# Optimization experiments

Measured on AMD Instinct MI355X. Metric: run time of the kernel, lower is better.

The kernel has to match this reference:

```python
import jax, jax.numpy as jnp
import numpy as np

T, D_IN, D_OUT, HEADS, FREQ = 2048, 1024, 1024, 8, 10000
DH = D_OUT // HEADS


def absolute_pos(t, d, freq):
    # AP[pos, 2i] = sin(pos / freq**(2i/d)), AP[pos, 2i+1] = cos(...); t even -> all cols filled
    pos = jnp.arange(t, dtype=jnp.float32)[:, None]            # [T,1]
    i = jnp.arange(t // 2, dtype=jnp.float32)[None, :]         # [1,T/2]
    angle = pos / (freq ** (2.0 * i / d))                      # [T,T/2]
    return jnp.stack([jnp.sin(angle), jnp.cos(angle)], axis=-1).reshape(t, t)


def setup_inputs() -> dict:
    key = jax.random.key(0)
    ks = jax.random.split(key, 6)
    s = 0.02
    return {
        "x": jax.random.normal(ks[0], (T, D_IN), jnp.float32),
        "Wq": jax.random.normal(ks[1], (HEADS, DH, D_IN), jnp.float32) * s,
        "Wk": jax.random.normal(ks[2], (HEADS, DH, D_IN), jnp.float32) * s,
        "Wv": jax.random.normal(ks[3], (HEADS, DH, D_IN), jnp.float32) * s,
        "Wout2": jax.random.normal(ks[4], (DH, DH + 2), jnp.float32) * s,
        "Wout": jax.random.normal(ks[5], (D_IN, D_OUT), jnp.float32) * s,
    }


def reference(x, Wq, Wk, Wv, Wout2, Wout):
    t = x.shape[0]
    # diversity = 1 - cosine similarity (F.normalize with eps=1e-12)
    x_unit = x / jnp.maximum(jnp.linalg.norm(x, axis=1, keepdims=True), 1e-12)
    diversity = 1.0 - x_unit @ x_unit.T                        # [T,T]

    # all heads vectorized; torch Linear weight is [out,in] -> x @ W.T
    Q = jnp.einsum('td,hed->hte', x, Wq)                       # [H,T,DH]
    K = jnp.einsum('td,hed->hte', x, Wk)
    V = jnp.einsum('td,hed->hte', x, Wv)

    AP = absolute_pos(t, D_IN, FREQ)                           # [T,T]
    energies = jnp.einsum('hte,hse->hts', Q, K) + AP           # [H,T,T]

    att = jax.nn.softmax(energies, axis=-1)
    logp = jax.nn.log_softmax(energies, axis=-1)
    entropy = -(att * logp).sum(-1) / np.float32(np.log(t))    # [H,T]
    entropy = entropy / jnp.maximum(jnp.abs(entropy).sum(-1, keepdims=True), 1e-12)

    # dep_factor[j] broadcast over rows: masked[i,j] = dep[j]*att[i,j]
    dep = (diversity[None] * att).sum(-1) / diversity.sum(-1)[None]  # [H,T]
    att_win = att + dep[:, None, :] * att                      # [H,T,T]

    # dropout(p=0.5) treated as identity (eval mode)
    y = jnp.einsum('hts,hse->hte', att_win, V)                 # [H,T,DH]

    chars = jax.lax.stop_gradient(jnp.stack([entropy, dep], axis=-1))  # [H,T,2]
    y_s = jnp.einsum('htf,of->hto', jnp.concatenate([y, chars], axis=-1), Wout2)  # [H,T,DH]

    y_cat = jnp.transpose(y_s, (1, 0, 2)).reshape(t, D_OUT)    # cat heads along feature dim
    out = y_cat @ Wout.T                                       # [T,D_IN]
    return out, att_win[-1]
```

## Files before the change

### kernel.cpp

```cpp
#include <hip/hip_runtime.h>
#include <math.h>

#define TT  2048
#define NH  8
#define DH  128
#define LNT 7.6246189861593985f

typedef unsigned short ushort_t;
typedef __bf16 bf16x8 __attribute__((ext_vector_type(8)));
typedef _Float16 f16x8 __attribute__((ext_vector_type(8)));
typedef float f32x4 __attribute__((ext_vector_type(4)));
typedef unsigned int uintx4 __attribute__((ext_vector_type(4)));

#define MFMA16(a, b, c)  __builtin_amdgcn_mfma_f32_16x16x32_bf16(a, b, c, 0, 0, 0)
#define MFMA16F(a, b, c) __builtin_amdgcn_mfma_f32_16x16x32_f16(a, b, c, 0, 0, 0)

__device__ __forceinline__ bf16x8 ld8(const ushort_t* p) {
  uintx4 v = *(const uintx4*)p;
  return __builtin_bit_cast(bf16x8, v);
}
__device__ __forceinline__ f16x8 ld8f(const ushort_t* p) {
  uintx4 v = *(const uintx4*)p;
  return __builtin_bit_cast(f16x8, v);
}
__device__ __forceinline__ ushort_t f2bf(float x) {
  unsigned u = __float_as_uint(x);
  return (ushort_t)((u + 0x7fffu + ((u >> 16) & 1u)) >> 16);
}
__device__ __forceinline__ float bf2f(ushort_t b) {
  return __uint_as_float(((unsigned)b) << 16);
}
__device__ __forceinline__ ushort_t f2h(float x) {
  return __builtin_bit_cast(ushort_t, (_Float16)x);
}
__device__ __forceinline__ float h2f(ushort_t b) {
  return (float)__builtin_bit_cast(_Float16, b);
}


enum : size_t {
  F_XF   = 0u,
  F_UF   = 1048576u,
  F_QF   = 2097152u,
  F_KF   = 3145728u,
  F_VBF  = 4194304u,
  F_VT   = 5242880u,
  F_YCF  = 6291456u,
  F_WCAT = 7340032u,
  F_WOF  = 9437184u,
  F_DIVS = 9961472u,
  F_LST  = 9979904u,
  F_ENTR = 9996288u,
  F_ENT  = 10012672u,
  F_DEP  = 10029056u,
  F_W2F  = 10307584u,
  F_APH  = 10485760u,
  F_C    = 12582912u,
  F_LP   = 6291456u,
  F_SAP  = 6422528u,
  F_SCP  = 6553600u,
  F_E    = 16777216u,
  F_YPALL= 33554432u,
  F_YSH  = 2097152u,
};

__device__ __forceinline__ float blockReduceSum256(float v) {
  __shared__ float sh[4];
  #pragma unroll
  for (int m = 1; m < 64; m <<= 1) v += __shfl_xor(v, m, 64);
  if ((threadIdx.x & 63) == 0) sh[threadIdx.x >> 6] = v;
  __syncthreads();
  float r = sh[0] + sh[1] + sh[2] + sh[3];
  __syncthreads();
  return r;
}

__global__ __launch_bounds__(256) void k_pre(
    const float* __restrict__ x, const float* __restrict__ Wq,
    const float* __restrict__ Wk, const float* __restrict__ Wv,
    const float* __restrict__ Wo, const float* __restrict__ W2,
    ushort_t* __restrict__ xf, ushort_t* __restrict__ Wcat,
    ushort_t* __restrict__ Wof, ushort_t* __restrict__ W2f,
    ushort_t* __restrict__ Uf, ushort_t* __restrict__ APf) {
  int b = blockIdx.x;
  if (b < 6240) {
    int i = b * 256 + threadIdx.x;
    if (i < 1572864) {
      const float* src; ushort_t* dst; int j;
      if (i < 524288)       { src = x;  dst = xf;             j = i; }
      else if (i < 786432)  { src = Wq; dst = Wcat;           j = i - 524288; }
      else if (i < 1048576) { src = Wk; dst = Wcat + 1048576; j = i - 786432; }
      else if (i < 1310720) { src = Wv; dst = Wcat + 2097152; j = i - 1048576; }
      else                  { src = Wo; dst = Wof;            j = i - 1310720; }
      float4 v = ((const float4*)src)[j];
      uint2 w;
      w.x = (unsigned)f2h(v.x) | ((unsigned)f2h(v.y) << 16);
      w.y = (unsigned)f2h(v.z) | ((unsigned)f2h(v.w) << 16);
      ((uint2*)dst)[j] = w;
    } else {
      int idx = i - 1572864;
      int o = idx / 192, c = idx % 192;
      W2f[idx] = (c < 130) ? f2h(W2[o * 130 + c]) : (ushort_t)0;
    }
  } else if (b < 8288) {
    int t = b - 6240;
    const float* xr = x + (size_t)t * 1024;
    float ss = 0.f;
    for (int d = threadIdx.x; d < 1024; d += 256) { float v = xr[d]; ss += v * v; }
    ss = blockReduceSum256(ss);
    float inv = 1.f / fmaxf(sqrtf(ss), 1e-12f);
    for (int d = threadIdx.x; d < 1024; d += 256)
      Uf[(size_t)t * 1024 + d] = f2h(xr[d] * inv);
  } else {
    int bb = b - 8288;
    int tile_t = bb >> 4, sub = bb & 15;
    int base = sub * 2048;
    for (int u0 = threadIdx.x; u0 < 2048; u0 += 256) {
      int u = base + u0;
      int tile_s = u >> 8, slot = u & 255;
      int lg = slot >> 6, l15 = (slot >> 2) & 15, r = slot & 3;
      int t = tile_t * 16 + lg * 4 + r;
      int s = tile_s * 16 + l15;
      int i = s >> 1;
      float invf = __expf((float)i * -0.017988946039016016f);
      float ang = (float)t * invf;
      APf[(size_t)tile_t * 32768 + u] = f2h((s & 1) ? cosf(ang) : sinf(ang));
    }
  }
}

template <int MODE>
__device__ __forceinline__ void gemm_tile(
    ushort_t* As, ushort_t* Bs,
    const ushort_t* A, const ushort_t* B,
    float* Df, ushort_t* Dh,
    ushort_t* Dq, ushort_t* Dk, ushort_t* Dv,
    int M, int N, int K, int m0, int n0) {
  int tid = threadIdx.x, lane = tid & 63, w = tid >> 6;
  int l15 = lane & 15, lg = lane >> 4;
  int wr = w >> 1, wc = w & 1;

  const ushort_t* ga[4];
  const ushort_t* gb[4];
  ushort_t* la[4];
  ushort_t* lb[4];
  #pragma unroll
  for (int j = 0; j < 4; j++) {
    int u = (4 * w + j) * 64 + lane;
    int row = u >> 3;
    int kc8 = (u & 7) ^ (row & 7);
    ga[j] = A + (size_t)(m0 + row) * K + kc8 * 8;
    gb[j] = B + (size_t)(n0 + row) * K + kc8 * 8;
    la[j] = As + (4 * w + j) * 512;
    lb[j] = Bs + (4 * w + j) * 512;
  }

  f32x4 acc[4][4];
  #pragma unroll
  for (int i = 0; i < 4; i++)
    #pragma unroll
    for (int ct = 0; ct < 4; ct++) acc[i][ct] = (f32x4)0.f;

  for (int k0 = 0; k0 < K; k0 += 64) {
    __syncthreads();
    #pragma unroll
    for (int j = 0; j < 4; j++) {
      __builtin_amdgcn_global_load_lds(
          (const __attribute__((address_space(1))) void*)(ga[j] + k0),
          (__attribute__((address_space(3))) void*)la[j], 16, 0, 0);
      __builtin_amdgcn_global_load_lds(
          (const __attribute__((address_space(1))) void*)(gb[j] + k0),
          (__attribute__((address_space(3))) void*)lb[j], 16, 0, 0);
    }
    __syncthreads();
    #pragma unroll
    for (int kc = 0; kc < 2; kc++) {
      f16x8 af[4], bfr[4];
      #pragma unroll
      for (int i = 0; i < 4; i++) {
        int ra = wr * 64 + i * 16 + l15;
        af[i] = ld8f(As + (ra * 8 + ((kc * 4 + lg) ^ (ra & 7))) * 8);
        int rb = wc * 64 + i * 16 + l15;
        bfr[i] = ld8f(Bs + (rb * 8 + ((kc * 4 + lg) ^ (rb & 7))) * 8);
      }
      #pragma unroll
      for (int i = 0; i < 4; i++)
        #pragma unroll
        for (int ct = 0; ct < 4; ct++)
          acc[i][ct] = MFMA16F(af[i], bfr[ct], acc[i][ct]);
    }
  }
  #pragma unroll
  for (int i = 0; i < 4; i++) {
    #pragma unroll
    for (int ct = 0; ct < 4; ct++) {
      if (MODE == 5) {
        size_t tile_t = (size_t)(m0 + wr * 64 + i * 16) >> 4;
        size_t tile_s = (size_t)(n0 + wc * 64 + ct * 16) >> 4;
        uint2 wv;
        wv.x = (unsigned)f2bf(acc[i][ct][0]) | ((unsigned)f2bf(acc[i][ct][1]) << 16);
        wv.y = (unsigned)f2bf(acc[i][ct][2]) | ((unsigned)f2bf(acc[i][ct][3]) << 16);
        *(uint2*)(Dh + (tile_t * (size_t)(N >> 4) + tile_s) * 256 + lg * 64 + l15 * 4) = wv;
      } else {
        #pragma unroll
        for (int r = 0; r < 4; r++) {
          size_t mm = m0 + wr * 64 + i * 16 + lg * 4 + r;
          size_t nn = n0 + wc * 64 + ct * 16 + l15;
          float v = acc[i][ct][r];
          if (MODE == 0) Df[mm * N + nn] = v;
          if (MODE == 3) {
            if (nn < 1024) Dq[mm * 1024 + nn] = f2h(v);
            else if (nn < 2048) Dk[mm * 1024 + nn - 1024] = f2h(v);
            else Dv[mm * 1024 + nn - 2048] = f2bf(v);
          }
          if (MODE == 4) {
            size_t hh = mm >> 11, tt2 = mm & 2047;
            Dh[tt2 * 1024 + hh * 128 + nn] = f2h(v);
          }
        }
      }
    }
  }
}

template <int MODE>
__global__ __launch_bounds__(256) void k_gemm(
    const ushort_t* __restrict__ A, const ushort_t* __restrict__ B,
    float* __restrict__ Df, ushort_t* __restrict__ Dh,
    int M, int N, int K) {
  __shared__ __align__(16) ushort_t As[128 * 64];
  __shared__ __align__(16) ushort_t Bs[128 * 64];
  gemm_tile<MODE>(As, Bs, A, B, Df, Dh, nullptr, nullptr, nullptr,
                  M, N, K, blockIdx.y * 128, blockIdx.x * 128);
}

__global__ __launch_bounds__(256) void k_cqkv(
    const ushort_t* __restrict__ Uf, const ushort_t* __restrict__ xf,
    const ushort_t* __restrict__ Wcat,
    ushort_t* __restrict__ Cf, ushort_t* __restrict__ Qf,
    ushort_t* __restrict__ Kf, ushort_t* __restrict__ Vbf) {
  __shared__ __align__(16) ushort_t As[128 * 64];
  __shared__ __align__(16) ushort_t Bs[128 * 64];
  int bid = blockIdx.x;
  if (bid < 256) {
    gemm_tile<5>(As, Bs, Uf, Uf, nullptr, Cf, nullptr, nullptr, nullptr,
                 TT, TT, 1024, (bid >> 4) * 128, (bid & 15) * 128);
  } else {
    int b = bid - 256;
    gemm_tile<3>(As, Bs, xf, Wcat, nullptr, nullptr, Qf, Kf, Vbf,
                 TT, 3072, 1024, (b / 24) * 128, (b % 24) * 128);
  }
}

__global__ __launch_bounds__(256) void k_divsumf(const ushort_t* __restrict__ Cf,
                                                 float* __restrict__ divsum) {
  int tile_t = blockIdx.x;
  int tid = threadIdx.x;
  #pragma unroll
  for (int lg = 0; lg < 4; lg++) {
    float rs0 = 0.f, rs1 = 0.f, rs2 = 0.f, rs3 = 0.f;
    for (int u = tid; u < 128 * 8; u += 256) {
      int tile_s = u >> 3, j = u & 7;
      uintx4 v = *(const uintx4*)(Cf + ((size_t)tile_t * 128 + tile_s) * 256 + lg * 64 + j * 8);
      rs0 += bf2f((ushort_t)(v[0] & 0xffffu)) + bf2f((ushort_t)(v[2] & 0xffffu));
      rs1 += bf2f((ushort_t)(v[0] >> 16))     + bf2f((ushort_t)(v[2] >> 16));
      rs2 += bf2f((ushort_t)(v[1] & 0xffffu)) + bf2f((ushort_t)(v[3] & 0xffffu));
      rs3 += bf2f((ushort_t)(v[1] >> 16))     + bf2f((ushort_t)(v[3] >> 16));
    }
    float t0 = blockReduceSum256(rs0);
    float t1 = blockReduceSum256(rs1);
    float t2 = blockReduceSum256(rs2);
    float t3 = blockReduceSum256(rs3);
    if (tid == 0) {
      divsum[tile_t * 16 + lg * 4 + 0] = (float)TT - t0;
      divsum[tile_t * 16 + lg * 4 + 1] = (float)TT - t1;
      divsum[tile_t * 16 + lg * 4 + 2] = (float)TT - t2;
      divsum[tile_t * 16 + lg * 4 + 3] = (float)TT - t3;
    }
  }
}

__global__ __launch_bounds__(512, 4) void k_phase1m(
    const ushort_t* __restrict__ Qf, const ushort_t* __restrict__ Kf,
    const ushort_t* __restrict__ APf, const ushort_t* __restrict__ Cf,
    ushort_t* __restrict__ Ef,
    float* __restrict__ Lp, float* __restrict__ sap, float* __restrict__ scp) {
  int h = blockIdx.y, z = blockIdx.z;
  int tid = threadIdx.x, lane = tid & 63, w = tid >> 6;
  int l15 = lane & 15, lg = lane >> 4;
  int rowbase = blockIdx.x * 128 + w * 16;
  int s_begin = z * 256, s_end = s_begin + 256;
  __shared__ __align__(16) ushort_t Ks[64 * 128];

  f16x8 q[4];
  {
    const ushort_t* qp = Qf + (size_t)(rowbase + l15) * 1024 + h * DH + lg * 8;
    #pragma unroll
    for (int kc = 0; kc < 4; kc++) q[kc] = ld8f(qp + kc * 32);
  }
  const ushort_t* apb = APf + (size_t)(rowbase >> 4) * 32768 + lane * 4;
  const ushort_t* cfb = Cf  + (size_t)(rowbase >> 4) * 32768 + lane * 4;
  ushort_t* eb = Ef + ((size_t)(h * 128 + (rowbase >> 4)) * 128) * 256 + lane * 4;

  int n0 = w * 128 + lane;
  int sr0 = n0 >> 4, su0 = n0 & 15, sr1 = sr0 + 4;
  int wo0 = sr0 * 128 + ((su0 ^ (sr0 & 7)) * 8);
  int wo1 = sr1 * 128 + ((su0 ^ (sr1 & 7)) * 8);
  const ushort_t* kg0 = Kf + (size_t)sr0 * 1024 + h * DH + su0 * 8;
  const ushort_t* kg1 = Kf + (size_t)sr1 * 1024 + h * DH + su0 * 8;

  float Lv[4], sae[4], snc[4];
  #pragma unroll
  for (int r = 0; r < 4; r++) { Lv[r] = 0.f; sae[r] = 0.f; snc[r] = 0.f; }

  uintx4 ka = *(const uintx4*)(kg0 + (size_t)s_begin * 1024);
  uintx4 kb = *(const uintx4*)(kg1 + (size_t)s_begin * 1024);

  for (int s0 = s_begin; s0 < s_end; s0 += 64) {
    int ts0 = s0 >> 4;
    f32x4 acc[4];
    float cc[4][4];
    #pragma unroll
    for (int ct = 0; ct < 4; ct++) {
      uint2 ap2 = *(const uint2*)(apb + (size_t)(ts0 + ct) * 256);
      uint2 c2  = *(const uint2*)(cfb + (size_t)(ts0 + ct) * 256);
      acc[ct][0] = h2f((ushort_t)(ap2.x & 0xffffu));
      acc[ct][1] = h2f((ushort_t)(ap2.x >> 16));
      acc[ct][2] = h2f((ushort_t)(ap2.y & 0xffffu));
      acc[ct][3] = h2f((ushort_t)(ap2.y >> 16));
      cc[ct][0] = bf2f((ushort_t)(c2.x & 0xffffu));
      cc[ct][1] = bf2f((ushort_t)(c2.x >> 16));
      cc[ct][2] = bf2f((ushort_t)(c2.y & 0xffffu));
      cc[ct][3] = bf2f((ushort_t)(c2.y >> 16));
    }
    __syncthreads();
    *(uintx4*)(Ks + wo0) = ka;
    *(uintx4*)(Ks + wo1) = kb;
    int s1 = s0 + 64;
    if (s1 < s_end) {
      ka = *(const uintx4*)(kg0 + (size_t)s1 * 1024);
      kb = *(const uintx4*)(kg1 + (size_t)s1 * 1024);
    }
    __syncthreads();
    #pragma unroll
    for (int ct = 0; ct < 4; ct++) {
      int row = ct * 16 + l15, rb = row * 128, rs = row & 7;
      #pragma unroll
      for (int kc = 0; kc < 4; kc++) {
        f16x8 b = ld8f(Ks + rb + (((kc * 4 + lg) ^ rs) * 8));
        acc[ct] = MFMA16F(q[kc], b, acc[ct]);
      }
    }
    #pragma unroll
    for (int ct = 0; ct < 4; ct++) {
      uint2 ev;
      ev.x = (unsigned)f2h(acc[ct][0]) | ((unsigned)f2h(acc[ct][1]) << 16);
      ev.y = (unsigned)f2h(acc[ct][2]) | ((unsigned)f2h(acc[ct][3]) << 16);
      *(uint2*)(eb + (size_t)(ts0 + ct) * 256) = ev;
    }
    #pragma unroll
    for (int r = 0; r < 4; r++) {
      float e0 = acc[0][r], e1 = acc[1][r], e2 = acc[2][r], e3 = acc[3][r];
      float p0 = __expf(e0), p1 = __expf(e1), p2 = __expf(e2), p3 = __expf(e3);
      Lv[r]  += (p0 + p1) + (p2 + p3);
      sae[r] += (p0 * e0 + p1 * e1) + (p2 * e2 + p3 * e3);
      snc[r] += (p0 * cc[0][r] + p1 * cc[1][r]) + (p2 * cc[2][r] + p3 * cc[3][r]);
    }
  }
  #pragma unroll
  for (int r = 0; r < 4; r++) {
    #pragma unroll
    for (int m = 1; m < 16; m <<= 1) {
      Lv[r]  += __shfl_xor(Lv[r], m, 64);
      sae[r] += __shfl_xor(sae[r], m, 64);
      snc[r] += __shfl_xor(snc[r], m, 64);
    }
  }
  if (l15 == 0) {
    #pragma unroll
    for (int r = 0; r < 4; r++) {
      int t = rowbase + lg * 4 + r;
      size_t idx = (size_t)z * (NH * TT) + h * TT + t;
      Lp[idx] = Lv[r]; sap[idx] = sae[r]; scp[idx] = snc[r];
    }
  }
}

__global__ __launch_bounds__(256) void k_combine(
    const float* __restrict__ Lp, const float* __restrict__ sap,
    const float* __restrict__ scp, const float* __restrict__ divsum,
    float* __restrict__ Lst, float* __restrict__ entraw, float* __restrict__ dep) {
  int i = blockIdx.x * 256 + threadIdx.x;
  if (i >= NH * TT) return;
  float L = 0.f, sa = 0.f, sc = 0.f;
  #pragma unroll
  for (int c = 0; c < 8; c++) {
    size_t idx = (size_t)c * (NH * TT) + i;
    L += Lp[idx]; sa += sap[idx]; sc += scp[idx];
  }
  float logL = __logf(L);
  Lst[i] = logL;
  entraw[i] = (logL - sa / L) * (1.0f / LNT);
  int t = i & (TT - 1);
  dep[i] = (1.f - sc / L) / divsum[t];
}

__global__ __launch_bounds__(256) void k_entnorm(const float* __restrict__ entraw,
                                                 float* __restrict__ ent) {
  int h = blockIdx.x;
  float s = 0.f;
  for (int t = threadIdx.x; t < TT; t += 256) s += fabsf(entraw[h * TT + t]);
  s = blockReduceSum256(s);
  float inv = 1.f / fmaxf(s, 1e-12f);
  for (int t = threadIdx.x; t < TT; t += 256) ent[h * TT + t] = entraw[h * TT + t] * inv;
}

__global__ __launch_bounds__(256) void k_vprime(const ushort_t* __restrict__ Vbf,
                                                const float* __restrict__ dep,
                                                ushort_t* __restrict__ VT) {
  int h = blockIdx.y, s0 = blockIdx.x * 64;
  __shared__ float tile[64][130];
  int tid = threadIdx.x;
  for (int idx = tid; idx < 64 * 64; idx += 256) {
    int r = idx >> 6, c2 = (idx & 63) * 2;
    unsigned u = *(const unsigned*)&Vbf[(size_t)(s0 + r) * 1024 + h * DH + c2];
    tile[r][c2] = bf2f((ushort_t)(u & 0xffffu));
    tile[r][c2 + 1] = bf2f((ushort_t)(u >> 16));
  }
  __syncthreads();
  int e = tid >> 1, sh = (tid & 1) * 32;
  #pragma unroll
  for (int g = 0; g < 8; g++) {
    int sb = sh + g * 4;
    float v0 = tile[sb + 0][e] * (1.f + dep[h * TT + s0 + sb + 0]);
    float v1 = tile[sb + 1][e] * (1.f + dep[h * TT + s0 + sb + 1]);
    float v2 = tile[sb + 2][e] * (1.f + dep[h * TT + s0 + sb + 2]);
    float v3 = tile[sb + 3][e] * (1.f + dep[h * TT + s0 + sb + 3]);
    uint2 wv;
    wv.x = (unsigned)f2bf(v0) | ((unsigned)f2bf(v1) << 16);
    wv.y = (unsigned)f2bf(v2) | ((unsigned)f2bf(v3) << 16);
    *(uint2*)&VT[(size_t)(h * DH + e) * TT + s0 + sb] = wv;
  }
}

__global__ __launch_bounds__(512, 4) void k_phase2m(
    const ushort_t* __restrict__ Ef, const ushort_t* __restrict__ VT,
    const float* __restrict__ Lst, const float* __restrict__ dep,
    ushort_t* __restrict__ ypall, float* __restrict__ out2) {
  int h = (blockIdx.y + 7) & 7;
  int z = blockIdx.z;
  int tid = threadIdx.x, lane = tid & 63, w = tid >> 6;
  int l15 = lane & 15, lg = lane >> 4;
  int rowbase = blockIdx.x * 128 + w * 16;
  bool last = (h == NH - 1);
  int s_begin = z * 256, s_end = s_begin + 256;
  ushort_t* yp = ypall + (size_t)z * 2097152;

  __shared__ __align__(16) ushort_t Vs[128 * 64];
  __shared__ __align__(16) ushort_t Pst[8][16][72];

  float ml[4];
  #pragma unroll
  for (int r = 0; r < 4; r++) ml[r] = Lst[h * TT + rowbase + lg * 4 + r];
  const ushort_t* eb = Ef + ((size_t)(h * 128 + (rowbase >> 4)) * 128) * 256 + lane * 4;

  int n0 = w * 128 + lane;
  int ve0 = n0 >> 3, vu0 = n0 & 7;
  int vwo0 = ve0 * 64 + ((vu0 ^ (ve0 & 7)) * 8);
  int vwo1 = vwo0 + 512;
  const ushort_t* vg0 = VT + (size_t)(h * DH + ve0) * TT + vu0 * 8;
  const ushort_t* vg1 = vg0 + (size_t)8 * TT;

  f32x4 yacc[8];
  #pragma unroll
  for (int et = 0; et < 8; et++) yacc[et] = (f32x4)0.f;

  uintx4 va = *(const uintx4*)(vg0 + s_begin);
  uintx4 vb = *(const uintx4*)(vg1 + s_begin);

  for (int s0 = s_begin; s0 < s_end; s0 += 64) {
    int ts0 = s0 >> 4;
    uint2 e2[4];
    #pragma unroll
    for (int ct = 0; ct < 4; ct++)
      e2[ct] = *(const uint2*)(eb + (size_t)(ts0 + ct) * 256);
    __syncthreads();
    *(uintx4*)(Vs + vwo0) = va;
    *(uintx4*)(Vs + vwo1) = vb;
    int s1 = s0 + 64;
    if (s1 < s_end) {
      va = *(const uintx4*)(vg0 + s1);
      vb = *(const uintx4*)(vg1 + s1);
    }
    __syncthreads();
    float dv[4];
    if (last) {
      #pragma unroll
      for (int ct = 0; ct < 4; ct++) dv[ct] = dep[(NH - 1) * TT + s0 + ct * 16 + l15];
    }
    #pragma unroll
    for (int ct = 0; ct < 4; ct++) {
      float e0 = h2f((ushort_t)(e2[ct].x & 0xffffu));
      float e1 = h2f((ushort_t)(e2[ct].x >> 16));
      float e3 = h2f((ushort_t)(e2[ct].y & 0xffffu));
      float e4 = h2f((ushort_t)(e2[ct].y >> 16));
      float a0 = __expf(e0 - ml[0]);
      float a1 = __expf(e1 - ml[1]);
      float a2 = __expf(e3 - ml[2]);
      float a3 = __expf(e4 - ml[3]);
      Pst[w][lg * 4 + 0][ct * 16 + l15] = f2bf(a0);
      Pst[w][lg * 4 + 1][ct * 16 + l15] = f2bf(a1);
      Pst[w][lg * 4 + 2][ct * 16 + l15] = f2bf(a2);
      Pst[w][lg * 4 + 3][ct * 16 + l15] = f2bf(a3);
      if (last) {
        float sc = 1.f + dv[ct];
        out2[(size_t)(rowbase + lg * 4 + 0) * TT + s0 + ct * 16 + l15] = a0 * sc;
        out2[(size_t)(rowbase + lg * 4 + 1) * TT + s0 + ct * 16 + l15] = a1 * sc;
        out2[(size_t)(rowbase + lg * 4 + 2) * TT + s0 + ct * 16 + l15] = a2 * sc;
        out2[(size_t)(rowbase + lg * 4 + 3) * TT + s0 + ct * 16 + l15] = a3 * sc;
      }
    }
    asm volatile("" ::: "memory");
    #pragma unroll
    for (int c = 0; c < 2; c++) {
      bf16x8 ap = *(const bf16x8*)&Pst[w][l15][c * 32 + lg * 8];
      #pragma unroll
      for (int et = 0; et < 8; et++) {
        int e = et * 16 + l15;
        bf16x8 bv = ld8(Vs + e * 64 + (((c * 4 + lg) ^ (l15 & 7)) * 8));
        yacc[et] = MFMA16(ap, bv, yacc[et]);
      }
    }
    asm volatile("" ::: "memory");
  }
  #pragma unroll
  for (int et = 0; et < 8; et++)
    #pragma unroll
    for (int r = 0; r < 4; r++)
      yp[((size_t)h * TT + rowbase + lg * 4 + r) * DH + et * 16 + l15] = f2h(yacc[et][r]);
}

__device__ __forceinline__ void acc8(const ushort_t* p, float* s) {
  uintx4 v = *(const uintx4*)p;
  #pragma unroll
  for (int q = 0; q < 4; q++) {
    s[q * 2]     += h2f((ushort_t)(v[q] & 0xffffu));
    s[q * 2 + 1] += h2f((ushort_t)(v[q] >> 16));
  }
}
__global__ __launch_bounds__(256) void k_ysum(
    const ushort_t* __restrict__ ypall,
    const float* __restrict__ ent, const float* __restrict__ dep,
    ushort_t* __restrict__ ysh) {
  int i = blockIdx.x * 256 + threadIdx.x;
  int g = i & 15, t = (i >> 4) & 2047, h = i >> 15;
  size_t src = ((size_t)h * TT + t) * DH + g * 8;
  float s[8];
  #pragma unroll
  for (int q = 0; q < 8; q++) s[q] = 0.f;
  #pragma unroll
  for (int b = 0; b < 8; b++) acc8(ypall + (size_t)b * 2097152 + src, s);
  uintx4 o;
  o[0] = (unsigned)f2h(s[0]) | ((unsigned)f2h(s[1]) << 16);
  o[1] = (unsigned)f2h(s[2]) | ((unsigned)f2h(s[3]) << 16);
  o[2] = (unsigned)f2h(s[4]) | ((unsigned)f2h(s[5]) << 16);
  o[3] = (unsigned)f2h(s[6]) | ((unsigned)f2h(s[7]) << 16);
  ushort_t* row = ysh + ((size_t)h * TT + t) * 192;
  *(uintx4*)(row + g * 8) = o;
  if (g == 0) {
    uint2 cz;
    cz.x = (unsigned)f2h(ent[h * TT + t]) | ((unsigned)f2h(dep[h * TT + t]) << 16);
    cz.y = 0u;
    *(uint2*)(row + 128) = cz;
    uint2 z2; z2.x = 0u; z2.y = 0u;
    #pragma unroll
    for (int q = 132; q < 192; q += 4) *(uint2*)(row + q) = z2;
  }
}

extern "C" void kernel_launch(void* const* d_in, const int* in_sizes, int n_in,
                              void* d_out, int out_size, void* d_ws, size_t ws_size,
                              hipStream_t stream) {
  const float* x  = (const float*)d_in[0];
  const float* Wq = (const float*)d_in[1];
  const float* Wk = (const float*)d_in[2];
  const float* Wv = (const float*)d_in[3];
  const float* W2 = (const float*)d_in[4];
  const float* Wo = (const float*)d_in[5];
  float* out  = (float*)d_out;
  float* out2 = out + (size_t)TT * 1024;
  float* ws = (float*)d_ws;

  ushort_t* xf   = (ushort_t*)(ws + F_XF);
  ushort_t* Uf   = (ushort_t*)(ws + F_UF);
  ushort_t* Qf   = (ushort_t*)(ws + F_QF);
  ushort_t* Kf   = (ushort_t*)(ws + F_KF);
  ushort_t* Vbf  = (ushort_t*)(ws + F_VBF);
  ushort_t* VT   = (ushort_t*)(ws + F_VT);
  ushort_t* ycf  = (ushort_t*)(ws + F_YCF);
  ushort_t* Wcat = (ushort_t*)(ws + F_WCAT);
  ushort_t* Wof  = (ushort_t*)(ws + F_WOF);
  ushort_t* W2f  = (ushort_t*)(ws + F_W2F);
  ushort_t* APf  = (ushort_t*)(ws + F_APH);
  ushort_t* ysh  = (ushort_t*)(ws + F_YSH);
  ushort_t* Cf   = (ushort_t*)(ws + F_C);
  ushort_t* Ef   = (ushort_t*)(ws + F_E);
  ushort_t* ypall= (ushort_t*)(ws + F_YPALL);
  float* divsum = ws + F_DIVS;
  float* Lst    = ws + F_LST;
  float* entraw = ws + F_ENTR;
  float* ent    = ws + F_ENT;
  float* dep    = ws + F_DEP;
  float* Lp     = ws + F_LP;
  float* sap    = ws + F_SAP;
  float* scp    = ws + F_SCP;

  k_pre<<<10336, 256, 0, stream>>>(x, Wq, Wk, Wv, Wo, W2,
                                   xf, Wcat, Wof, W2f, Uf, APf);
  k_cqkv<<<640, 256, 0, stream>>>(Uf, xf, Wcat, Cf, Qf, Kf, Vbf);
  k_divsumf<<<128, 256, 0, stream>>>(Cf, divsum);

  k_phase1m<<<dim3(16, NH, 8), 512, 0, stream>>>(Qf, Kf, APf, Cf, Ef, Lp, sap, scp);
  k_combine<<<64, 256, 0, stream>>>(Lp, sap, scp, divsum, Lst, entraw, dep);
  k_entnorm<<<NH, 256, 0, stream>>>(entraw, ent);
  k_vprime<<<dim3(32, NH), 256, 0, stream>>>(Vbf, dep, VT);
  k_phase2m<<<dim3(16, NH, 8), 512, 0, stream>>>(Ef, VT, Lst, dep, ypall, out2);
  k_ysum<<<1024, 256, 0, stream>>>(ypall, ent, dep, ysh);
  k_gemm<4><<<dim3(1, 128), 256, 0, stream>>>(ysh, W2f, nullptr, ycf, 16384, 128, 192);
  k_gemm<0><<<dim3(8, 16), 256, 0, stream>>>(ycf, Wof, out, nullptr, TT, 1024, 1024);
}
```

Baseline: 174.1 us.

## Store unnormalized exp scores in phase1 and fuse diversity row sums into GEMM epilogue

Phase 1 now writes exp(energy) as bf16 instead of raw fp16 energies. Phase 2 therefore skips the second exponential and just copies these values into shared memory, applying 1/L once to the output accumulator and to the last-head attention output. The separate divsum kernel is removed: k_pre initialises divsum to T, and the cosine-similarity GEMM epilogue subtracts row sums atomically. This drops a kernel launch and a pass over C, but relies on unnormalized exp not overflowing bf16, and atomics make the summation order nondeterministic.

```diff
diff --git a/kernel.cpp b/kernel.cpp
--- a/kernel.cpp
+++ b/kernel.cpp
@@ -49,17 +49,17 @@
   F_WCAT = 7340032u,
   F_WOF  = 9437184u,
   F_DIVS = 9961472u,
-  F_LST  = 9979904u,
   F_ENTR = 9996288u,
   F_ENT  = 10012672u,
   F_DEP  = 10029056u,
+  F_LINV = 10045440u,
   F_W2F  = 10307584u,
   F_APH  = 10485760u,
   F_C    = 12582912u,
   F_LP   = 6291456u,
   F_SAP  = 6422528u,
   F_SCP  = 6553600u,
-  F_E    = 16777216u,
+  F_P    = 16777216u,
   F_YPALL= 33554432u,
   F_YSH  = 2097152u,
 };
@@ -81,7 +81,8 @@
     const float* __restrict__ Wo, const float* __restrict__ W2,
     ushort_t* __restrict__ xf, ushort_t* __restrict__ Wcat,
     ushort_t* __restrict__ Wof, ushort_t* __restrict__ W2f,
-    ushort_t* __restrict__ Uf, ushort_t* __restrict__ APf) {
+    ushort_t* __restrict__ Uf, ushort_t* __restrict__ APf,
+    float* __restrict__ divsum) {
   int b = blockIdx.x;
   if (b < 6240) {
     int i = b * 256 + threadIdx.x;
@@ -111,7 +112,7 @@
     float inv = 1.f / fmaxf(sqrtf(ss), 1e-12f);
     for (int d = threadIdx.x; d < 1024; d += 256)
       Uf[(size_t)t * 1024 + d] = f2h(xr[d] * inv);
-  } else {
+  } else if (b < 10336) {
     int bb = b - 8288;
     int tile_t = bb >> 4, sub = bb & 15;
     int base = sub * 2048;
@@ -126,6 +127,9 @@
       float ang = (float)t * invf;
       APf[(size_t)tile_t * 32768 + u] = f2h((s & 1) ? cosf(ang) : sinf(ang));
     }
+  } else {
+    int idx = (b - 10336) * 256 + threadIdx.x;
+    if (idx < TT) divsum[idx] = (float)TT;
   }
 }
 
@@ -192,15 +196,20 @@
   }
   #pragma unroll
   for (int i = 0; i < 4; i++) {
+    float rs[4] = {0.f, 0.f, 0.f, 0.f};
     #pragma unroll
     for (int ct = 0; ct < 4; ct++) {
-      if (MODE == 5) {
+      if (MODE == 5 || MODE == 6) {
         size_t tile_t = (size_t)(m0 + wr * 64 + i * 16) >> 4;
         size_t tile_s = (size_t)(n0 + wc * 64 + ct * 16) >> 4;
         uint2 wv;
         wv.x = (unsigned)f2bf(acc[i][ct][0]) | ((unsigned)f2bf(acc[i][ct][1]) << 16);
         wv.y = (unsigned)f2bf(acc[i][ct][2]) | ((unsigned)f2bf(acc[i][ct][3]) << 16);
         *(uint2*)(Dh + (tile_t * (size_t)(N >> 4) + tile_s) * 256 + lg * 64 + l15 * 4) = wv;
+        if (MODE == 6) {
+          rs[0] += acc[i][ct][0]; rs[1] += acc[i][ct][1];
+          rs[2] += acc[i][ct][2]; rs[3] += acc[i][ct][3];
+        }
       } else {
         #pragma unroll
         for (int r = 0; r < 4; r++) {
@@ -220,6 +229,16 @@
         }
       }
     }
+    if (MODE == 6) {
+      #pragma unroll
+      for (int r = 0; r < 4; r++) {
+        float s = rs[r];
+        s += __shfl_xor(s, 1, 64); s += __shfl_xor(s, 2, 64);
+        s += __shfl_xor(s, 4, 64); s += __shfl_xor(s, 8, 64);
+        if (l15 == 0)
+          atomicAdd(&Df[m0 + wr * 64 + i * 16 + lg * 4 + r], -s);
+      }
+    }
   }
 }
 
@@ -238,12 +257,13 @@
     const ushort_t* __restrict__ Uf, const ushort_t* __restrict__ xf,
     const ushort_t* __restrict__ Wcat,
     ushort_t* __restrict__ Cf, ushort_t* __restrict__ Qf,
-    ushort_t* __restrict__ Kf, ushort_t* __restrict__ Vbf) {
+    ushort_t* __restrict__ Kf, ushort_t* __restrict__ Vbf,
+    float* __restrict__ divsum) {
   __shared__ __align__(16) ushort_t As[128 * 64];
   __shared__ __align__(16) ushort_t Bs[128 * 64];
   int bid = blockIdx.x;
   if (bid < 256) {
-    gemm_tile<5>(As, Bs, Uf, Uf, nullptr, Cf, nullptr, nullptr, nullptr,
+    gemm_tile<6>(As, Bs, Uf, Uf, divsum, Cf, nullptr, nullptr, nullptr,
                  TT, TT, 1024, (bid >> 4) * 128, (bid & 15) * 128);
   } else {
     int b = bid - 256;
@@ -252,38 +272,10 @@
   }
 }
 
-__global__ __launch_bounds__(256) void k_divsumf(const ushort_t* __restrict__ Cf,
-                                                 float* __restrict__ divsum) {
-  int tile_t = blockIdx.x;
-  int tid = threadIdx.x;
-  #pragma unroll
-  for (int lg = 0; lg < 4; lg++) {
-    float rs0 = 0.f, rs1 = 0.f, rs2 = 0.f, rs3 = 0.f;
-    for (int u = tid; u < 128 * 8; u += 256) {
-      int tile_s = u >> 3, j = u & 7;
-      uintx4 v = *(const uintx4*)(Cf + ((size_t)tile_t * 128 + tile_s) * 256 + lg * 64 + j * 8);
-      rs0 += bf2f((ushort_t)(v[0] & 0xffffu)) + bf2f((ushort_t)(v[2] & 0xffffu));
-      rs1 += bf2f((ushort_t)(v[0] >> 16))     + bf2f((ushort_t)(v[2] >> 16));
-      rs2 += bf2f((ushort_t)(v[1] & 0xffffu)) + bf2f((ushort_t)(v[3] & 0xffffu));
-      rs3 += bf2f((ushort_t)(v[1] >> 16))     + bf2f((ushort_t)(v[3] >> 16));
-    }
-    float t0 = blockReduceSum256(rs0);
-    float t1 = blockReduceSum256(rs1);
-    float t2 = blockReduceSum256(rs2);
-    float t3 = blockReduceSum256(rs3);
-    if (tid == 0) {
-      divsum[tile_t * 16 + lg * 4 + 0] = (float)TT - t0;
-      divsum[tile_t * 16 + lg * 4 + 1] = (float)TT - t1;
-      divsum[tile_t * 16 + lg * 4 + 2] = (float)TT - t2;
-      divsum[tile_t * 16 + lg * 4 + 3] = (float)TT - t3;
-    }
-  }
-}
-
 __global__ __launch_bounds__(512, 4) void k_phase1m(
     const ushort_t* __restrict__ Qf, const ushort_t* __restrict__ Kf,
     const ushort_t* __restrict__ APf, const ushort_t* __restrict__ Cf,
-    ushort_t* __restrict__ Ef,
+    ushort_t* __restrict__ Pf,
     float* __restrict__ Lp, float* __restrict__ sap, float* __restrict__ scp) {
   int h = blockIdx.y, z = blockIdx.z;
   int tid = threadIdx.x, lane = tid & 63, w = tid >> 6;
@@ -300,7 +292,7 @@
   }
   const ushort_t* apb = APf + (size_t)(rowbase >> 4) * 32768 + lane * 4;
   const ushort_t* cfb = Cf  + (size_t)(rowbase >> 4) * 32768 + lane * 4;
-  ushort_t* eb = Ef + ((size_t)(h * 128 + (rowbase >> 4)) * 128) * 256 + lane * 4;
+  ushort_t* pb = Pf + ((size_t)(h * 128 + (rowbase >> 4)) * 128) * 256 + lane * 4;
 
   int n0 = w * 128 + lane;
   int sr0 = n0 >> 4, su0 = n0 & 15, sr1 = sr0 + 4;
@@ -344,27 +336,30 @@
     __syncthreads();
     #pragma unroll
     for (int ct = 0; ct < 4; ct++) {
-      int row = ct * 16 + l15, rb = row * 128, rs = row & 7;
+      int row = ct * 16 + l15, rb = row * 128, rsw = row & 7;
       #pragma unroll
       for (int kc = 0; kc < 4; kc++) {
-        f16x8 b = ld8f(Ks + rb + (((kc * 4 + lg) ^ rs) * 8));
+        f16x8 b = ld8f(Ks + rb + (((kc * 4 + lg) ^ rsw) * 8));
         acc[ct] = MFMA16F(q[kc], b, acc[ct]);
       }
     }
+    float pz[4][4];
     #pragma unroll
     for (int ct = 0; ct < 4; ct++) {
-      uint2 ev;
-      ev.x = (unsigned)f2h(acc[ct][0]) | ((unsigned)f2h(acc[ct][1]) << 16);
-      ev.y = (unsigned)f2h(acc[ct][2]) | ((unsigned)f2h(acc[ct][3]) << 16);
-      *(uint2*)(eb + (size_t)(ts0 + ct) * 256) = ev;
+      #pragma unroll
+      for (int r = 0; r < 4; r++) pz[ct][r] = __expf(acc[ct][r]);
+      uint2 pv;
+      pv.x = (unsigned)f2bf(pz[ct][0]) | ((unsigned)f2bf(pz[ct][1]) << 16);
+      pv.y = (unsigned)f2bf(pz[ct][2]) | ((unsigned)f2bf(pz[ct][3]) << 16);
+      *(uint2*)(pb + (size_t)(ts0 + ct) * 256) = pv;
     }
     #pragma unroll
     for (int r = 0; r < 4; r++) {
-      float e0 = acc[0][r], e1 = acc[1][r], e2 = acc[2][r], e3 = acc[3][r];
-      float p0 = __expf(e0), p1 = __expf(e1), p2 = __expf(e2), p3 = __expf(e3);
-      Lv[r]  += (p0 + p1) + (p2 + p3);
-      sae[r] += (p0 * e0 + p1 * e1) + (p2 * e2 + p3 * e3);
-      snc[r] += (p0 * cc[0][r] + p1 * cc[1][r]) + (p2 * cc[2][r] + p3 * cc[3][r]);
+      Lv[r]  += (pz[0][r] + pz[1][r]) + (pz[2][r] + pz[3][r]);
+      sae[r] += (pz[0][r] * acc[0][r] + pz[1][r] * acc[1][r]) +
+                (pz[2][r] * acc[2][r] + pz[3][r] * acc[3][r]);
+      snc[r] += (pz[0][r] * cc[0][r] + pz[1][r] * cc[1][r]) +
+                (pz[2][r] * cc[2][r] + pz[3][r] * cc[3][r]);
     }
   }
   #pragma unroll
@@ -389,7 +384,7 @@
 __global__ __launch_bounds__(256) void k_combine(
     const float* __restrict__ Lp, const float* __restrict__ sap,
     const float* __restrict__ scp, const float* __restrict__ divsum,
-    float* __restrict__ Lst, float* __restrict__ entraw, float* __restrict__ dep) {
+    float* __restrict__ Linv, float* __restrict__ entraw, float* __restrict__ dep) {
   int i = blockIdx.x * 256 + threadIdx.x;
   if (i >= NH * TT) return;
   float L = 0.f, sa = 0.f, sc = 0.f;
@@ -399,7 +394,7 @@
     L += Lp[idx]; sa += sap[idx]; sc += scp[idx];
   }
   float logL = __logf(L);
-  Lst[i] = logL;
+  Linv[i] = 1.f / L;
   entraw[i] = (logL - sa / L) * (1.0f / LNT);
   int t = i & (TT - 1);
   dep[i] = (1.f - sc / L) / divsum[t];
@@ -444,8 +439,8 @@
 }
 
 __global__ __launch_bounds__(512, 4) void k_phase2m(
-    const ushort_t* __restrict__ Ef, const ushort_t* __restrict__ VT,
-    const float* __restrict__ Lst, const float* __restrict__ dep,
+    const ushort_t* __restrict__ Pf, const ushort_t* __restrict__ VT,
+    const float* __restrict__ Linv, const float* __restrict__ dep,
     ushort_t* __restrict__ ypall, float* __restrict__ out2) {
   int h = (blockIdx.y + 7) & 7;
   int z = blockIdx.z;
@@ -459,10 +454,10 @@
   __shared__ __align__(16) ushort_t Vs[128 * 64];
   __shared__ __align__(16) ushort_t Pst[8][16][72];
 
-  float ml[4];
-  #pragma unroll
-  for (int r = 0; r < 4; r++) ml[r] = Lst[h * TT + rowbase + lg * 4 + r];
-  const ushort_t* eb = Ef + ((size_t)(h * 128 + (rowbase >> 4)) * 128) * 256 + lane * 4;
+  float il[4];
+  #pragma unroll
+  for (int r = 0; r < 4; r++) il[r] = Linv[h * TT + rowbase + lg * 4 + r];
+  const ushort_t* pb = Pf + ((size_t)(h * 128 + (rowbase >> 4)) * 128) * 256 + lane * 4;
 
   int n0 = w * 128 + lane;
   int ve0 = n0 >> 3, vu0 = n0 & 7;
@@ -480,10 +475,10 @@
 
   for (int s0 = s_begin; s0 < s_end; s0 += 64) {
     int ts0 = s0 >> 4;
-    uint2 e2[4];
+    uint2 p2[4];
     #pragma unroll
     for (int ct = 0; ct < 4; ct++)
-      e2[ct] = *(const uint2*)(eb + (size_t)(ts0 + ct) * 256);
+      p2[ct] = *(const uint2*)(pb + (size_t)(ts0 + ct) * 256);
     __syncthreads();
     *(uintx4*)(Vs + vwo0) = va;
     *(uintx4*)(Vs + vwo1) = vb;
@@ -493,31 +488,22 @@
       vb = *(const uintx4*)(vg1 + s1);
     }
     __syncthreads();
-    float dv[4];
-    if (last) {
-      #pragma unroll
-      for (int ct = 0; ct < 4; ct++) dv[ct] = dep[(NH - 1) * TT + s0 + ct * 16 + l15];
-    }
     #pragma unroll
     for (int ct = 0; ct < 4; ct++) {
-      float e0 = h2f((ushort_t)(e2[ct].x & 0xffffu));
-      float e1 = h2f((ushort_t)(e2[ct].x >> 16));
-      float e3 = h2f((ushort_t)(e2[ct].y & 0xffffu));
-      float e4 = h2f((ushort_t)(e2[ct].y >> 16));
-      float a0 = __expf(e0 - ml[0]);
-      float a1 = __expf(e1 - ml[1]);
-      float a2 = __expf(e3 - ml[2]);
-      float a3 = __expf(e4 - ml[3]);
-      Pst[w][lg * 4 + 0][ct * 16 + l15] = f2bf(a0);
-      Pst[w][lg * 4 + 1][ct * 16 + l15] = f2bf(a1);
-      Pst[w][lg * 4 + 2][ct * 16 + l15] = f2bf(a2);
-      Pst[w][lg * 4 + 3][ct * 16 + l15] = f2bf(a3);
+      ushort_t p0 = (ushort_t)(p2[ct].x & 0xffffu);
+      ushort_t p1 = (ushort_t)(p2[ct].x >> 16);
+      ushort_t p3 = (ushort_t)(p2[ct].y & 0xffffu);
+      ushort_t p4 = (ushort_t)(p2[ct].y >> 16);
+      Pst[w][lg * 4 + 0][ct * 16 + l15] = p0;
+      Pst[w][lg * 4 + 1][ct * 16 + l15] = p1;
+      Pst[w][lg * 4 + 2][ct * 16 + l15] = p3;
+      Pst[w][lg * 4 + 3][ct * 16 + l15] = p4;
       if (last) {
-        float sc = 1.f + dv[ct];
-        out2[(size_t)(rowbase + lg * 4 + 0) * TT + s0 + ct * 16 + l15] = a0 * sc;
-        out2[(size_t)(rowbase + lg * 4 + 1) * TT + s0 + ct * 16 + l15] = a1 * sc;
-        out2[(size_t)(rowbase + lg * 4 + 2) * TT + s0 + ct * 16 + l15] = a2 * sc;
-        out2[(size_t)(rowbase + lg * 4 + 3) * TT + s0 + ct * 16 + l15] = a3 * sc;
+        float sc = (1.f + dep[(NH - 1) * TT + s0 + ct * 16 + l15]);
+        out2[(size_t)(rowbase + lg * 4 + 0) * TT + s0 + ct * 16 + l15] = bf2f(p0) * il[0] * sc;
+        out2[(size_t)(rowbase + lg * 4 + 1) * TT + s0 + ct * 16 + l15] = bf2f(p1) * il[1] * sc;
+        out2[(size_t)(rowbase + lg * 4 + 2) * TT + s0 + ct * 16 + l15] = bf2f(p3) * il[2] * sc;
+        out2[(size_t)(rowbase + lg * 4 + 3) * TT + s0 + ct * 16 + l15] = bf2f(p4) * il[3] * sc;
       }
     }
     asm volatile("" ::: "memory");
@@ -537,7 +523,8 @@
   for (int et = 0; et < 8; et++)
     #pragma unroll
     for (int r = 0; r < 4; r++)
-      yp[((size_t)h * TT + rowbase + lg * 4 + r) * DH + et * 16 + l15] = f2h(yacc[et][r]);
+      yp[((size_t)h * TT + rowbase + lg * 4 + r) * DH + et * 16 + l15] =
+          f2h(yacc[et][r] * il[r]);
 }
 
 __device__ __forceinline__ void acc8(const ushort_t* p, float* s) {
@@ -604,10 +591,10 @@
   ushort_t* APf  = (ushort_t*)(ws + F_APH);
   ushort_t* ysh  = (ushort_t*)(ws + F_YSH);
   ushort_t* Cf   = (ushort_t*)(ws + F_C);
-  ushort_t* Ef   = (ushort_t*)(ws + F_E);
+  ushort_t* Pf   = (ushort_t*)(ws + F_P);
   ushort_t* ypall= (ushort_t*)(ws + F_YPALL);
   float* divsum = ws + F_DIVS;
-  float* Lst    = ws + F_LST;
+  float* Linv   = ws + F_LINV;
   float* entraw = ws + F_ENTR;
   float* ent    = ws + F_ENT;
   float* dep    = ws + F_DEP;
@@ -615,16 +602,15 @@
   float* sap    = ws + F_SAP;
   float* scp    = ws + F_SCP;
 
-  k_pre<<<10336, 256, 0, stream>>>(x, Wq, Wk, Wv, Wo, W2,
-                                   xf, Wcat, Wof, W2f, Uf, APf);
-  k_cqkv<<<640, 256, 0, stream>>>(Uf, xf, Wcat, Cf, Qf, Kf, Vbf);
-  k_divsumf<<<128, 256, 0, stream>>>(Cf, divsum);
-
-  k_phase1m<<<dim3(16, NH, 8), 512, 0, stream>>>(Qf, Kf, APf, Cf, Ef, Lp, sap, scp);
-  k_combine<<<64, 256, 0, stream>>>(Lp, sap, scp, divsum, Lst, entraw, dep);
+  k_pre<<<10344, 256, 0, stream>>>(x, Wq, Wk, Wv, Wo, W2,
+                                   xf, Wcat, Wof, W2f, Uf, APf, divsum);
+  k_cqkv<<<640, 256, 0, stream>>>(Uf, xf, Wcat, Cf, Qf, Kf, Vbf, divsum);
+
+  k_phase1m<<<dim3(16, NH, 8), 512, 0, stream>>>(Qf, Kf, APf, Cf, Pf, Lp, sap, scp);
+  k_combine<<<64, 256, 0, stream>>>(Lp, sap, scp, divsum, Linv, entraw, dep);
   k_entnorm<<<NH, 256, 0, stream>>>(entraw, ent);
   k_vprime<<<dim3(32, NH), 256, 0, stream>>>(Vbf, dep, VT);
-  k_phase2m<<<dim3(16, NH, 8), 512, 0, stream>>>(Ef, VT, Lst, dep, ypall, out2);
+  k_phase2m<<<dim3(16, NH, 8), 512, 0, stream>>>(Pf, VT, Linv, dep, ypall, out2);
   k_ysum<<<1024, 256, 0, stream>>>(ypall, ent, dep, ysh);
   k_gemm<4><<<dim3(1, 128), 256, 0, stream>>>(ysh, W2f, nullptr, ycf, 16384, 128, 192);
   k_gemm<0><<<dim3(8, 16), 256, 0, stream>>>(ycf, Wof, out, nullptr, TT, 1024, 1024);
```

New measurement: 194.8 us. +11.9%, slower.
